# Kernel tuning notes

Hardware: AMD Instinct MI355X
Metric: run time of the kernel (lower is better)

The kernel has to match this reference:

```python
import jax, jax.numpy as jnp
import numpy as np
import jax.lax as lax

B, S, E, H = 8, 4096, 1024, 128
TAU = 1.0
MIN_K = 32

def setup_inputs() -> dict:
    key = jax.random.key(0)
    k0, k1, k2, k3 = jax.random.split(key, 4)
    token_embeddings = jax.random.normal(k0, (B, S, E), dtype=jnp.float32)
    w1 = jax.random.normal(k1, (E, H), dtype=jnp.float32) * (1.0 / np.sqrt(E))
    b1 = jnp.zeros((H,), dtype=jnp.float32)
    w2 = jax.random.normal(k2, (H, 1), dtype=jnp.float32) * (1.0 / np.sqrt(H))
    b2 = jnp.zeros((1,), dtype=jnp.float32)
    # uniform noise for Gumbel, same bounds as the original module
    u = jax.random.uniform(k3, (B, S), minval=1e-08, maxval=1.0 - 1e-08, dtype=jnp.float32)
    return {"token_embeddings": token_embeddings, "w1": w1, "b1": b1, "w2": w2, "b2": b2, "u": u}

def reference(token_embeddings, w1, b1, w2, b2, u):
    # scorer MLP: Dense(H) -> relu -> Dense(1), squeeze -> [B, S]
    h = jax.nn.relu(jnp.einsum('bse,eh->bsh', token_embeddings, w1) + b1)
    importance_logits = (jnp.einsum('bsh,ho->bso', h, w2) + b2)[..., 0]  # [B, S]

    # expected_k (value_function is None): soft count of kept tokens
    expected_k = jax.nn.sigmoid(importance_logits).sum(axis=-1)  # [B]
    k = jnp.clip(expected_k.astype(jnp.int32), MIN_K, None)      # [B]

    # Gumbel-softmax top-k, hard=True
    gumbel = -jnp.log(-jnp.log(u))
    soft_mask = jax.nn.softmax((importance_logits + gumbel) / TAU, axis=-1)  # [B, S]

    # hard mask: 1.0 at the top-k[i] positions of soft_mask per row.
    # Equivalent to the original argsort + while_loop scatter: positions with
    # descending-sort rank < k[i] get 1.0.
    order = jnp.argsort(-soft_mask, axis=-1)          # [B, S] descending order
    ranks = jnp.argsort(order, axis=-1)               # rank of each position
    hard_mask = (ranks < k[:, None]).astype(soft_mask.dtype)

    selection_mask = lax.stop_gradient(hard_mask - soft_mask) + soft_mask
    filtered_embeddings = token_embeddings * selection_mask[..., None]
    return filtered_embeddings, selection_mask, expected_k
```

## Files before the change

kernel.cpp:

```cpp
#include <hip/hip_runtime.h>
#include <hip/hip_bf16.h>
#include <math.h>

#define B_ 8
#define S_ 4096
#define E_ 1024
#define H_ 128
#define MIN_K 32
#define OUT_MASK_OFF (B_*S_*E_)
#define OUT_EK_OFF   (B_*S_*E_ + B_*S_)

#define LOGITS_OFF 0
#define SOFT_OFF   131072
#define CNT_OFF    262144
#define KROW_OFF   393216
#define W1T_HI_OFF 393248
#define W1T_LO_OFF 655392

typedef __attribute__((ext_vector_type(8))) short   frag8;
typedef __attribute__((ext_vector_type(4))) float   fragc;
typedef __attribute__((ext_vector_type(4))) unsigned short us4;

static __device__ __forceinline__ unsigned short bf16_rne(float f) {
  unsigned u = __float_as_uint(f);
  unsigned r = u + 0x7FFF + ((u >> 16) & 1);
  return (unsigned short)(r >> 16);
}
static __device__ __forceinline__ float bf16_to_f32(unsigned short h) {
  return __uint_as_float(((unsigned)h) << 16);
}

__global__ __launch_bounds__(256) void prep_w_kernel(
    const float* __restrict__ w1,
    unsigned short* __restrict__ w1t_hi, unsigned short* __restrict__ w1t_lo)
{
  int id = blockIdx.x * 256 + threadIdx.x;
  int k  = id >> 5;
  int n4 = id & 31;
  float4 w = *(const float4*)(w1 + k * H_ + n4 * 4);
#pragma unroll
  for (int e = 0; e < 4; ++e) {
    float f = (e == 0) ? w.x : (e == 1) ? w.y : (e == 2) ? w.z : w.w;
    unsigned short hi = bf16_rne(f);
    unsigned short lo = bf16_rne(f - bf16_to_f32(hi));
    int n = n4 * 4 + e;
    w1t_hi[n * E_ + k] = hi;
    w1t_lo[n * E_ + k] = lo;
  }
}

#define KT 32
#define XS_STRIDE 40
#define NTILES (E_ / KT)

__global__ __launch_bounds__(256, 4) void scorer_kernel(
    const float* __restrict__ x,
    const unsigned short* __restrict__ w1t_hi,
    const unsigned short* __restrict__ w1t_lo,
    const float* __restrict__ b1, const float* __restrict__ w2,
    const float* __restrict__ b2, float* __restrict__ logits)
{
  __shared__ unsigned short xs_hi[2][32 * XS_STRIDE];
  __shared__ unsigned short xs_lo[2][32 * XS_STRIDE];
  __shared__ float part[4][32];

  const int tid  = threadIdx.x;
  const int wave = tid >> 6;
  const int lane = tid & 63;
  const int l15  = lane & 15;
  const int quad = lane >> 4;
  const int m0   = blockIdx.x * 32;
  const int nbase = wave * 32;

  fragc acc[2][2];
#pragma unroll
  for (int mt = 0; mt < 2; ++mt)
#pragma unroll
    for (int nt = 0; nt < 2; ++nt)
      acc[mt][nt] = (fragc)(0.f);

  const int sm = tid >> 3, skq = tid & 7;
  const float* xrow = x + (size_t)(m0 + sm) * E_ + skq * 4;

  float4 pa = *(const float4*)(xrow);
  float4 pb = *(const float4*)(xrow + KT);

  frag8 bh[2], bl[2], bhn[2], bln[2];
#pragma unroll
  for (int nt = 0; nt < 2; ++nt) {
    int n = nbase + nt * 16 + l15;
    size_t off = (size_t)n * E_ + quad * 8;
    bh[nt] = *(const frag8*)(w1t_hi + off);
    bl[nt] = *(const frag8*)(w1t_lo + off);
  }

#pragma unroll 2
  for (int t = 0; t < NTILES; ++t) {
    const int buf = t & 1;
    {
      us4 h4, l4;
      float fv[4] = {pa.x, pa.y, pa.z, pa.w};
#pragma unroll
      for (int e = 0; e < 4; ++e) {
        unsigned short hi = bf16_rne(fv[e]);
        h4[e] = hi; l4[e] = bf16_rne(fv[e] - bf16_to_f32(hi));
      }
      *(us4*)&xs_hi[buf][sm * XS_STRIDE + skq * 4] = h4;
      *(us4*)&xs_lo[buf][sm * XS_STRIDE + skq * 4] = l4;
    }
    __syncthreads();

    pa = pb;
    if (t + 2 < NTILES)
      pb = *(const float4*)(xrow + (t + 2) * KT);
    if (t + 1 < NTILES) {
#pragma unroll
      for (int nt = 0; nt < 2; ++nt) {
        int n = nbase + nt * 16 + l15;
        size_t off = (size_t)n * E_ + (t + 1) * KT + quad * 8;
        bhn[nt] = *(const frag8*)(w1t_hi + off);
        bln[nt] = *(const frag8*)(w1t_lo + off);
      }
    }

    frag8 ah[2], al[2];
#pragma unroll
    for (int mt = 0; mt < 2; ++mt) {
      int a = (mt * 16 + l15) * XS_STRIDE + quad * 8;
      ah[mt] = *(const frag8*)&xs_hi[buf][a];
      al[mt] = *(const frag8*)&xs_lo[buf][a];
    }
#pragma unroll
    for (int mt = 0; mt < 2; ++mt)
#pragma unroll
      for (int nt = 0; nt < 2; ++nt) {
        acc[mt][nt] = __builtin_amdgcn_mfma_f32_16x16x32_bf16(ah[mt], bh[nt], acc[mt][nt], 0, 0, 0);
        acc[mt][nt] = __builtin_amdgcn_mfma_f32_16x16x32_bf16(ah[mt], bl[nt], acc[mt][nt], 0, 0, 0);
        acc[mt][nt] = __builtin_amdgcn_mfma_f32_16x16x32_bf16(al[mt], bh[nt], acc[mt][nt], 0, 0, 0);
      }
#pragma unroll
    for (int nt = 0; nt < 2; ++nt) { bh[nt] = bhn[nt]; bl[nt] = bln[nt]; }
  }

  float b1v[2], w2v[2];
#pragma unroll
  for (int nt = 0; nt < 2; ++nt) {
    int n = nbase + nt * 16 + l15;
    b1v[nt] = b1[n]; w2v[nt] = w2[n];
  }
  float v[2][4];
#pragma unroll
  for (int mt = 0; mt < 2; ++mt)
#pragma unroll
    for (int reg = 0; reg < 4; ++reg) {
      float p = 0.f;
#pragma unroll
      for (int nt = 0; nt < 2; ++nt) {
        float h = acc[mt][nt][reg] + b1v[nt];
        h = h > 0.f ? h : 0.f;
        p = fmaf(h, w2v[nt], p);
      }
      v[mt][reg] = p;
    }
#pragma unroll
  for (int mask = 1; mask < 16; mask <<= 1)
#pragma unroll
    for (int mt = 0; mt < 2; ++mt)
#pragma unroll
      for (int reg = 0; reg < 4; ++reg)
        v[mt][reg] += __shfl_xor(v[mt][reg], mask);

  if (l15 == 0) {
#pragma unroll
    for (int mt = 0; mt < 2; ++mt)
#pragma unroll
      for (int reg = 0; reg < 4; ++reg)
        part[wave][mt * 16 + quad * 4 + reg] = v[mt][reg];
  }
  __syncthreads();
  if (tid < 32)
    logits[m0 + tid] = ((part[0][tid] + part[1][tid]) + (part[2][tid] + part[3][tid])) + b2[0];
}

__global__ __launch_bounds__(1024) void row_kernel(
    const float* __restrict__ logits, const float* __restrict__ u,
    float* __restrict__ soft, int* __restrict__ krow, float* __restrict__ ek_out)
{
  const int b = blockIdx.x;
  const int t = threadIdx.x;
  const float* Lrow = logits + b * S_;
  const float* urow = u + b * S_;

  __shared__ double red[1024];
  __shared__ float  redf[1024];

  float z[4];
  double psig = 0.0;
  float zmax = -INFINITY;
#pragma unroll
  for (int i = 0; i < 4; ++i) {
    int j = t + i * 1024;
    float L = Lrow[j];
    float g = -logf(-logf(urow[j]));
    z[i] = L + g;
    psig += (double)(1.f / (1.f + expf(-L)));
    zmax = fmaxf(zmax, z[i]);
  }
  red[t] = psig; redf[t] = zmax;
  __syncthreads();
  for (int s2 = 512; s2 > 0; s2 >>= 1) {
    if (t < s2) { red[t] += red[t + s2]; redf[t] = fmaxf(redf[t], redf[t + s2]); }
    __syncthreads();
  }
  __shared__ float m_sh; __shared__ double ek_sh;
  if (t == 0) { m_sh = redf[0]; ek_sh = red[0]; }
  __syncthreads();
  float m = m_sh;

  float e[4];
  double pexp = 0.0;
#pragma unroll
  for (int i = 0; i < 4; ++i) { e[i] = expf(z[i] - m); pexp += (double)e[i]; }
  red[t] = pexp;
  __syncthreads();
  for (int s2 = 512; s2 > 0; s2 >>= 1) {
    if (t < s2) red[t] += red[t + s2];
    __syncthreads();
  }
  __shared__ float den_sh;
  if (t == 0) den_sh = (float)red[0];
  __syncthreads();
  float den = den_sh;
#pragma unroll
  for (int i = 0; i < 4; ++i) soft[b * S_ + t + i * 1024] = e[i] / den;

  if (t == 0) {
    float ekf = (float)ek_sh;
    int k = (int)ekf;
    if (k < MIN_K) k = MIN_K;
    krow[b] = k;
    ek_out[b] = ekf;
  }
}

__global__ __launch_bounds__(256) void rank_kernel(
    const float* __restrict__ soft, int* __restrict__ counts)
{
  __shared__ float4 sjs[256];
  const int b  = blockIdx.z;
  const int ic = blockIdx.x;
  const int jc = blockIdx.y;
  const int tid = threadIdx.x;
  const float* row = soft + b * S_;

  sjs[tid] = ((const float4*)row)[jc * 256 + tid];
  const int i = ic * 256 + tid;
  const float si = row[i];
  __syncthreads();

  int cnt = 0;
  const int jbase = jc * 1024;
  for (int j4 = 0; j4 < 256; ++j4) {
    float4 vv = sjs[j4];
    int j = jbase + j4 * 4;
    cnt += (vv.x > si) || (vv.x == si && (j + 0) < i);
    cnt += (vv.y > si) || (vv.y == si && (j + 1) < i);
    cnt += (vv.z > si) || (vv.z == si && (j + 2) < i);
    cnt += (vv.w > si) || (vv.w == si && (j + 3) < i);
  }
  atomicAdd(&counts[b * S_ + i], cnt);
}

__global__ __launch_bounds__(256) void filter_kernel(
    const float* __restrict__ x, const float* __restrict__ soft,
    const int* __restrict__ counts, const int* __restrict__ krow,
    float* __restrict__ out, float* __restrict__ mask_out)
{
  const int token = blockIdx.x;
  const int b = token >> 12;
  const float s = soft[token];
  const float h = (counts[token] < krow[b]) ? 1.f : 0.f;
  const float sel = (h - s) + s;

  size_t base = (size_t)token * (E_ / 4) + threadIdx.x;
  float4 v = ((const float4*)x)[base];
  v.x *= sel; v.y *= sel; v.z *= sel; v.w *= sel;
  ((float4*)out)[base] = v;
  if (threadIdx.x == 0) mask_out[token] = sel;
}

extern "C" void kernel_launch(void* const* d_in, const int* in_sizes, int n_in,
                              void* d_out, int out_size, void* d_ws, size_t ws_size,
                              hipStream_t stream) {
  const float* x  = (const float*)d_in[0];
  const float* w1 = (const float*)d_in[1];
  const float* b1 = (const float*)d_in[2];
  const float* w2 = (const float*)d_in[3];
  const float* b2 = (const float*)d_in[4];
  const float* u  = (const float*)d_in[5];

  float* out = (float*)d_out;
  float* out_filt = out;
  float* out_mask = out + OUT_MASK_OFF;
  float* out_ek   = out + OUT_EK_OFF;

  char* ws = (char*)d_ws;
  float*          ws_logits = (float*)(ws + LOGITS_OFF);
  float*          ws_soft   = (float*)(ws + SOFT_OFF);
  int*            ws_cnt    = (int*)(ws + CNT_OFF);
  int*            ws_krow   = (int*)(ws + KROW_OFF);
  unsigned short* ws_w1thi  = (unsigned short*)(ws + W1T_HI_OFF);
  unsigned short* ws_w1tlo  = (unsigned short*)(ws + W1T_LO_OFF);

  hipMemsetAsync(ws_cnt, 0, B_ * S_ * sizeof(int), stream);
  prep_w_kernel<<<dim3(128), dim3(256), 0, stream>>>(w1, ws_w1thi, ws_w1tlo);
  scorer_kernel<<<dim3(B_ * S_ / 32), dim3(256), 0, stream>>>(
      x, ws_w1thi, ws_w1tlo, b1, w2, b2, ws_logits);
  row_kernel<<<dim3(B_), dim3(1024), 0, stream>>>(ws_logits, u, ws_soft, ws_krow, out_ek);
  rank_kernel<<<dim3(16, 4, 8), dim3(256), 0, stream>>>(ws_soft, ws_cnt);
  filter_kernel<<<dim3(B_ * S_), dim3(256), 0, stream>>>(
      x, ws_soft, ws_cnt, ws_krow, out_filt, out_mask);
}
```

Baseline: 351.4 us.

## Load scorer A fragments directly to registers and enlarge block tile to 64 rows

The scorer GEMM no longer stages x through shared memory with a per-tile barrier. Each wave loads its own A fragments from global memory into registers, splits them into bf16 hi/lo parts in place, and double-buffers A and B fragments in registers. The block tile grows to 64 rows with a 2x2 wave layout, so each wave computes 32x64 and reuses each B fragment across two M tiles. The aim is to remove LDS traffic and barriers and improve operand reuse, at the cost of more registers (occupancy lowered to 2), redundant hi/lo conversion in each N-half wave, and less coalesced strided global loads for x.

```diff
diff --git a/kernel.cpp b/kernel.cpp
--- a/kernel.cpp
+++ b/kernel.cpp
@@ -19,7 +19,6 @@
 
 typedef __attribute__((ext_vector_type(8))) short   frag8;
 typedef __attribute__((ext_vector_type(4))) float   fragc;
-typedef __attribute__((ext_vector_type(4))) unsigned short us4;
 
 static __device__ __forceinline__ unsigned short bf16_rne(float f) {
   unsigned u = __float_as_uint(f);
@@ -50,105 +49,108 @@
 }
 
 #define KT 32
-#define XS_STRIDE 40
 #define NTILES (E_ / KT)
 
-__global__ __launch_bounds__(256, 4) void scorer_kernel(
+__global__ __launch_bounds__(256, 2) void scorer_kernel(
     const float* __restrict__ x,
     const unsigned short* __restrict__ w1t_hi,
     const unsigned short* __restrict__ w1t_lo,
     const float* __restrict__ b1, const float* __restrict__ w2,
     const float* __restrict__ b2, float* __restrict__ logits)
 {
-  __shared__ unsigned short xs_hi[2][32 * XS_STRIDE];
-  __shared__ unsigned short xs_lo[2][32 * XS_STRIDE];
-  __shared__ float part[4][32];
+  __shared__ float part[2][4][32];
 
   const int tid  = threadIdx.x;
-  const int wave = tid >> 6;
+  const int wv   = tid >> 6;
   const int lane = tid & 63;
   const int l15  = lane & 15;
   const int quad = lane >> 4;
-  const int m0   = blockIdx.x * 32;
-  const int nbase = wave * 32;
-
-  fragc acc[2][2];
+  const int mh   = wv >> 1;
+  const int nh   = wv & 1;
+  const int m0   = blockIdx.x * 64;
+
+  const float* __restrict__ ar[2];
 #pragma unroll
   for (int mt = 0; mt < 2; ++mt)
-#pragma unroll
-    for (int nt = 0; nt < 2; ++nt)
+    ar[mt] = x + (size_t)(m0 + mh * 32 + mt * 16 + l15) * E_ + quad * 8;
+
+  const unsigned short* __restrict__ bhp[4];
+  const unsigned short* __restrict__ blp[4];
+#pragma unroll
+  for (int nt = 0; nt < 4; ++nt) {
+    size_t off = (size_t)(nh * 64 + nt * 16 + l15) * E_ + quad * 8;
+    bhp[nt] = w1t_hi + off;
+    blp[nt] = w1t_lo + off;
+  }
+
+  fragc acc[2][4];
+#pragma unroll
+  for (int mt = 0; mt < 2; ++mt)
+#pragma unroll
+    for (int nt = 0; nt < 4; ++nt)
       acc[mt][nt] = (fragc)(0.f);
 
-  const int sm = tid >> 3, skq = tid & 7;
-  const float* xrow = x + (size_t)(m0 + sm) * E_ + skq * 4;
-
-  float4 pa = *(const float4*)(xrow);
-  float4 pb = *(const float4*)(xrow + KT);
-
-  frag8 bh[2], bl[2], bhn[2], bln[2];
-#pragma unroll
-  for (int nt = 0; nt < 2; ++nt) {
-    int n = nbase + nt * 16 + l15;
-    size_t off = (size_t)n * E_ + quad * 8;
-    bh[nt] = *(const frag8*)(w1t_hi + off);
-    bl[nt] = *(const frag8*)(w1t_lo + off);
+  float4 Ax[2][2][2];
+  frag8  Bh[2][4], Bl[2][4];
+
+#pragma unroll
+  for (int mt = 0; mt < 2; ++mt) {
+    Ax[0][mt][0] = *(const float4*)(ar[mt] + 0);
+    Ax[0][mt][1] = *(const float4*)(ar[mt] + 4);
+  }
+#pragma unroll
+  for (int nt = 0; nt < 4; ++nt) {
+    Bh[0][nt] = *(const frag8*)(bhp[nt]);
+    Bl[0][nt] = *(const frag8*)(blp[nt]);
   }
 
 #pragma unroll 2
   for (int t = 0; t < NTILES; ++t) {
-    const int buf = t & 1;
-    {
-      us4 h4, l4;
-      float fv[4] = {pa.x, pa.y, pa.z, pa.w};
-#pragma unroll
-      for (int e = 0; e < 4; ++e) {
-        unsigned short hi = bf16_rne(fv[e]);
-        h4[e] = hi; l4[e] = bf16_rne(fv[e] - bf16_to_f32(hi));
-      }
-      *(us4*)&xs_hi[buf][sm * XS_STRIDE + skq * 4] = h4;
-      *(us4*)&xs_lo[buf][sm * XS_STRIDE + skq * 4] = l4;
+    const int cur = t & 1;
+    const int nxt = cur ^ 1;
+    const int kn = (t + 1 < NTILES) ? (t + 1) * KT : 0;
+
+#pragma unroll
+    for (int mt = 0; mt < 2; ++mt) {
+      Ax[nxt][mt][0] = *(const float4*)(ar[mt] + kn);
+      Ax[nxt][mt][1] = *(const float4*)(ar[mt] + kn + 4);
     }
-    __syncthreads();
-
-    pa = pb;
-    if (t + 2 < NTILES)
-      pb = *(const float4*)(xrow + (t + 2) * KT);
-    if (t + 1 < NTILES) {
-#pragma unroll
-      for (int nt = 0; nt < 2; ++nt) {
-        int n = nbase + nt * 16 + l15;
-        size_t off = (size_t)n * E_ + (t + 1) * KT + quad * 8;
-        bhn[nt] = *(const frag8*)(w1t_hi + off);
-        bln[nt] = *(const frag8*)(w1t_lo + off);
-      }
+#pragma unroll
+    for (int nt = 0; nt < 4; ++nt) {
+      Bh[nxt][nt] = *(const frag8*)(bhp[nt] + kn);
+      Bl[nxt][nt] = *(const frag8*)(blp[nt] + kn);
     }
 
     frag8 ah[2], al[2];
 #pragma unroll
     for (int mt = 0; mt < 2; ++mt) {
-      int a = (mt * 16 + l15) * XS_STRIDE + quad * 8;
-      ah[mt] = *(const frag8*)&xs_hi[buf][a];
-      al[mt] = *(const frag8*)&xs_lo[buf][a];
+      float f[8] = {Ax[cur][mt][0].x, Ax[cur][mt][0].y, Ax[cur][mt][0].z, Ax[cur][mt][0].w,
+                    Ax[cur][mt][1].x, Ax[cur][mt][1].y, Ax[cur][mt][1].z, Ax[cur][mt][1].w};
+#pragma unroll
+      for (int e = 0; e < 8; ++e) {
+        unsigned short hi = bf16_rne(f[e]);
+        ah[mt][e] = (short)hi;
+        al[mt][e] = (short)bf16_rne(f[e] - bf16_to_f32(hi));
+      }
     }
+
 #pragma unroll
     for (int mt = 0; mt < 2; ++mt)
 #pragma unroll
-      for (int nt = 0; nt < 2; ++nt) {
-        acc[mt][nt] = __builtin_amdgcn_mfma_f32_16x16x32_bf16(ah[mt], bh[nt], acc[mt][nt], 0, 0, 0);
-        acc[mt][nt] = __builtin_amdgcn_mfma_f32_16x16x32_bf16(ah[mt], bl[nt], acc[mt][nt], 0, 0, 0);
-        acc[mt][nt] = __builtin_amdgcn_mfma_f32_16x16x32_bf16(al[mt], bh[nt], acc[mt][nt], 0, 0, 0);
-      }
-#pragma unroll
-    for (int nt = 0; nt < 2; ++nt) { bh[nt] = bhn[nt]; bl[nt] = bln[nt]; }
-  }
-
-  float b1v[2], w2v[2];
-#pragma unroll
-  for (int nt = 0; nt < 2; ++nt) {
-    int n = nbase + nt * 16 + l15;
+      for (int nt = 0; nt < 4; ++nt) {
+        acc[mt][nt] = __builtin_amdgcn_mfma_f32_16x16x32_bf16(ah[mt], Bh[cur][nt], acc[mt][nt], 0, 0, 0);
+        acc[mt][nt] = __builtin_amdgcn_mfma_f32_16x16x32_bf16(ah[mt], Bl[cur][nt], acc[mt][nt], 0, 0, 0);
+        acc[mt][nt] = __builtin_amdgcn_mfma_f32_16x16x32_bf16(al[mt], Bh[cur][nt], acc[mt][nt], 0, 0, 0);
+      }
+  }
+
+  float b1v[4], w2v[4];
+#pragma unroll
+  for (int nt = 0; nt < 4; ++nt) {
+    int n = nh * 64 + nt * 16 + l15;
     b1v[nt] = b1[n]; w2v[nt] = w2[n];
   }
-  float v[2][4];
+  float pA[2][4], pB[2][4];
 #pragma unroll
   for (int mt = 0; mt < 2; ++mt)
 #pragma unroll
@@ -160,26 +162,42 @@
         h = h > 0.f ? h : 0.f;
         p = fmaf(h, w2v[nt], p);
       }
-      v[mt][reg] = p;
+      pA[mt][reg] = p;
+      p = 0.f;
+#pragma unroll
+      for (int nt = 2; nt < 4; ++nt) {
+        float h = acc[mt][nt][reg] + b1v[nt];
+        h = h > 0.f ? h : 0.f;
+        p = fmaf(h, w2v[nt], p);
+      }
+      pB[mt][reg] = p;
     }
 #pragma unroll
   for (int mask = 1; mask < 16; mask <<= 1)
 #pragma unroll
     for (int mt = 0; mt < 2; ++mt)
 #pragma unroll
-      for (int reg = 0; reg < 4; ++reg)
-        v[mt][reg] += __shfl_xor(v[mt][reg], mask);
+      for (int reg = 0; reg < 4; ++reg) {
+        pA[mt][reg] += __shfl_xor(pA[mt][reg], mask);
+        pB[mt][reg] += __shfl_xor(pB[mt][reg], mask);
+      }
 
   if (l15 == 0) {
 #pragma unroll
     for (int mt = 0; mt < 2; ++mt)
 #pragma unroll
-      for (int reg = 0; reg < 4; ++reg)
-        part[wave][mt * 16 + quad * 4 + reg] = v[mt][reg];
-  }
-  __syncthreads();
-  if (tid < 32)
-    logits[m0 + tid] = ((part[0][tid] + part[1][tid]) + (part[2][tid] + part[3][tid])) + b2[0];
+      for (int reg = 0; reg < 4; ++reg) {
+        int rl = mt * 16 + quad * 4 + reg;
+        part[mh][nh * 2 + 0][rl] = pA[mt][reg];
+        part[mh][nh * 2 + 1][rl] = pB[mt][reg];
+      }
+  }
+  __syncthreads();
+  if (tid < 64) {
+    int rmh = tid >> 5, rl = tid & 31;
+    logits[m0 + tid] = ((part[rmh][0][rl] + part[rmh][1][rl]) +
+                        (part[rmh][2][rl] + part[rmh][3][rl])) + b2[0];
+  }
 }
 
 __global__ __launch_bounds__(1024) void row_kernel(
@@ -314,7 +332,7 @@
 
   hipMemsetAsync(ws_cnt, 0, B_ * S_ * sizeof(int), stream);
   prep_w_kernel<<<dim3(128), dim3(256), 0, stream>>>(w1, ws_w1thi, ws_w1tlo);
-  scorer_kernel<<<dim3(B_ * S_ / 32), dim3(256), 0, stream>>>(
+  scorer_kernel<<<dim3(B_ * S_ / 64), dim3(256), 0, stream>>>(
       x, ws_w1thi, ws_w1tlo, b1, w2, b2, ws_logits);
   row_kernel<<<dim3(B_), dim3(1024), 0, stream>>>(ws_logits, u, ws_soft, ws_krow, out_ek);
   rank_kernel<<<dim3(16, 4, 8), dim3(256), 0, stream>>>(ws_soft, ws_cnt);
```

New measurement: 382.0 us. 1.09x slower.

## Load A fragments directly from global memory, drop LDS staging and barriers

Applied to the files above, without the earlier changes.

The scorer kernel no longer stages the fp32 embedding tile through double-buffered shared memory. Each wave now loads its own A fragments straight from global memory into registers and splits them into bf16 hi/lo parts there, which removes the per-tile __syncthreads and the LDS write/read traffic. The explicit register prefetch of the next tile is also dropped in favour of a simple non-unrolled loop. In exchange, all four waves redundantly load and convert the same 32x1024 x tile (4x global/L2 traffic and conversion work), and latency hiding now relies on occupancy rather than software pipelining.

```diff
diff --git a/kernel.cpp b/kernel.cpp
--- a/kernel.cpp
+++ b/kernel.cpp
@@ -19,7 +19,6 @@
 
 typedef __attribute__((ext_vector_type(8))) short   frag8;
 typedef __attribute__((ext_vector_type(4))) float   fragc;
-typedef __attribute__((ext_vector_type(4))) unsigned short us4;
 
 static __device__ __forceinline__ unsigned short bf16_rne(float f) {
   unsigned u = __float_as_uint(f);
@@ -50,7 +49,6 @@
 }
 
 #define KT 32
-#define XS_STRIDE 40
 #define NTILES (E_ / KT)
 
 __global__ __launch_bounds__(256, 4) void scorer_kernel(
@@ -60,108 +58,83 @@
     const float* __restrict__ b1, const float* __restrict__ w2,
     const float* __restrict__ b2, float* __restrict__ logits)
 {
-  __shared__ unsigned short xs_hi[2][32 * XS_STRIDE];
-  __shared__ unsigned short xs_lo[2][32 * XS_STRIDE];
   __shared__ float part[4][32];
 
   const int tid  = threadIdx.x;
-  const int wave = tid >> 6;
+  const int nh   = tid >> 6;
   const int lane = tid & 63;
   const int l15  = lane & 15;
   const int quad = lane >> 4;
   const int m0   = blockIdx.x * 32;
-  const int nbase = wave * 32;
-
-  fragc acc[2][2];
-#pragma unroll
-  for (int mt = 0; mt < 2; ++mt)
-#pragma unroll
-    for (int nt = 0; nt < 2; ++nt)
-      acc[mt][nt] = (fragc)(0.f);
-
-  const int sm = tid >> 3, skq = tid & 7;
-  const float* xrow = x + (size_t)(m0 + sm) * E_ + skq * 4;
-
-  float4 pa = *(const float4*)(xrow);
-  float4 pb = *(const float4*)(xrow + KT);
-
-  frag8 bh[2], bl[2], bhn[2], bln[2];
-#pragma unroll
-  for (int nt = 0; nt < 2; ++nt) {
-    int n = nbase + nt * 16 + l15;
-    size_t off = (size_t)n * E_ + quad * 8;
-    bh[nt] = *(const frag8*)(w1t_hi + off);
-    bl[nt] = *(const frag8*)(w1t_lo + off);
-  }
-
-#pragma unroll 2
+
+  const float* __restrict__ ar0 = x + (size_t)(m0 + 0  + l15) * E_ + quad * 8;
+  const float* __restrict__ ar1 = x + (size_t)(m0 + 16 + l15) * E_ + quad * 8;
+
+  const size_t bo0 = (size_t)(nh * 32 + 0  + l15) * E_ + quad * 8;
+  const size_t bo1 = (size_t)(nh * 32 + 16 + l15) * E_ + quad * 8;
+  const unsigned short* __restrict__ bh0p = w1t_hi + bo0;
+  const unsigned short* __restrict__ bh1p = w1t_hi + bo1;
+  const unsigned short* __restrict__ bl0p = w1t_lo + bo0;
+  const unsigned short* __restrict__ bl1p = w1t_lo + bo1;
+
+  fragc acc00 = (fragc)(0.f), acc01 = (fragc)(0.f);
+  fragc acc10 = (fragc)(0.f), acc11 = (fragc)(0.f);
+
+#pragma unroll 1
   for (int t = 0; t < NTILES; ++t) {
-    const int buf = t & 1;
+    const int k = t * KT;
+
+    float4 a00 = *(const float4*)(ar0 + k);
+    float4 a01 = *(const float4*)(ar0 + k + 4);
+    float4 a10 = *(const float4*)(ar1 + k);
+    float4 a11 = *(const float4*)(ar1 + k + 4);
+    frag8 bh0 = *(const frag8*)(bh0p + k);
+    frag8 bh1 = *(const frag8*)(bh1p + k);
+    frag8 bl0 = *(const frag8*)(bl0p + k);
+    frag8 bl1 = *(const frag8*)(bl1p + k);
+
+    frag8 ah0, al0, ah1, al1;
     {
-      us4 h4, l4;
-      float fv[4] = {pa.x, pa.y, pa.z, pa.w};
-#pragma unroll
-      for (int e = 0; e < 4; ++e) {
-        unsigned short hi = bf16_rne(fv[e]);
-        h4[e] = hi; l4[e] = bf16_rne(fv[e] - bf16_to_f32(hi));
-      }
-      *(us4*)&xs_hi[buf][sm * XS_STRIDE + skq * 4] = h4;
-      *(us4*)&xs_lo[buf][sm * XS_STRIDE + skq * 4] = l4;
-    }
-    __syncthreads();
-
-    pa = pb;
-    if (t + 2 < NTILES)
-      pb = *(const float4*)(xrow + (t + 2) * KT);
-    if (t + 1 < NTILES) {
-#pragma unroll
-      for (int nt = 0; nt < 2; ++nt) {
-        int n = nbase + nt * 16 + l15;
-        size_t off = (size_t)n * E_ + (t + 1) * KT + quad * 8;
-        bhn[nt] = *(const frag8*)(w1t_hi + off);
-        bln[nt] = *(const frag8*)(w1t_lo + off);
+      float f0[8] = {a00.x, a00.y, a00.z, a00.w, a01.x, a01.y, a01.z, a01.w};
+      float f1[8] = {a10.x, a10.y, a10.z, a10.w, a11.x, a11.y, a11.z, a11.w};
+#pragma unroll
+      for (int e = 0; e < 8; ++e) {
+        unsigned short hi0 = bf16_rne(f0[e]);
+        ah0[e] = (short)hi0;
+        al0[e] = (short)bf16_rne(f0[e] - bf16_to_f32(hi0));
+        unsigned short hi1 = bf16_rne(f1[e]);
+        ah1[e] = (short)hi1;
+        al1[e] = (short)bf16_rne(f1[e] - bf16_to_f32(hi1));
       }
     }
 
-    frag8 ah[2], al[2];
-#pragma unroll
-    for (int mt = 0; mt < 2; ++mt) {
-      int a = (mt * 16 + l15) * XS_STRIDE + quad * 8;
-      ah[mt] = *(const frag8*)&xs_hi[buf][a];
-      al[mt] = *(const frag8*)&xs_lo[buf][a];
-    }
-#pragma unroll
-    for (int mt = 0; mt < 2; ++mt)
-#pragma unroll
-      for (int nt = 0; nt < 2; ++nt) {
-        acc[mt][nt] = __builtin_amdgcn_mfma_f32_16x16x32_bf16(ah[mt], bh[nt], acc[mt][nt], 0, 0, 0);
-        acc[mt][nt] = __builtin_amdgcn_mfma_f32_16x16x32_bf16(ah[mt], bl[nt], acc[mt][nt], 0, 0, 0);
-        acc[mt][nt] = __builtin_amdgcn_mfma_f32_16x16x32_bf16(al[mt], bh[nt], acc[mt][nt], 0, 0, 0);
-      }
-#pragma unroll
-    for (int nt = 0; nt < 2; ++nt) { bh[nt] = bhn[nt]; bl[nt] = bln[nt]; }
-  }
-
-  float b1v[2], w2v[2];
-#pragma unroll
-  for (int nt = 0; nt < 2; ++nt) {
-    int n = nbase + nt * 16 + l15;
-    b1v[nt] = b1[n]; w2v[nt] = w2[n];
-  }
+    acc00 = __builtin_amdgcn_mfma_f32_16x16x32_bf16(ah0, bh0, acc00, 0, 0, 0);
+    acc00 = __builtin_amdgcn_mfma_f32_16x16x32_bf16(ah0, bl0, acc00, 0, 0, 0);
+    acc00 = __builtin_amdgcn_mfma_f32_16x16x32_bf16(al0, bh0, acc00, 0, 0, 0);
+    acc01 = __builtin_amdgcn_mfma_f32_16x16x32_bf16(ah0, bh1, acc01, 0, 0, 0);
+    acc01 = __builtin_amdgcn_mfma_f32_16x16x32_bf16(ah0, bl1, acc01, 0, 0, 0);
+    acc01 = __builtin_amdgcn_mfma_f32_16x16x32_bf16(al0, bh1, acc01, 0, 0, 0);
+    acc10 = __builtin_amdgcn_mfma_f32_16x16x32_bf16(ah1, bh0, acc10, 0, 0, 0);
+    acc10 = __builtin_amdgcn_mfma_f32_16x16x32_bf16(ah1, bl0, acc10, 0, 0, 0);
+    acc10 = __builtin_amdgcn_mfma_f32_16x16x32_bf16(al1, bh0, acc10, 0, 0, 0);
+    acc11 = __builtin_amdgcn_mfma_f32_16x16x32_bf16(ah1, bh1, acc11, 0, 0, 0);
+    acc11 = __builtin_amdgcn_mfma_f32_16x16x32_bf16(ah1, bl1, acc11, 0, 0, 0);
+    acc11 = __builtin_amdgcn_mfma_f32_16x16x32_bf16(al1, bh1, acc11, 0, 0, 0);
+  }
+
+  float b1v0 = b1[nh * 32 + 0  + l15], w2v0 = w2[nh * 32 + 0  + l15];
+  float b1v1 = b1[nh * 32 + 16 + l15], w2v1 = w2[nh * 32 + 16 + l15];
+
   float v[2][4];
 #pragma unroll
-  for (int mt = 0; mt < 2; ++mt)
-#pragma unroll
-    for (int reg = 0; reg < 4; ++reg) {
-      float p = 0.f;
-#pragma unroll
-      for (int nt = 0; nt < 2; ++nt) {
-        float h = acc[mt][nt][reg] + b1v[nt];
-        h = h > 0.f ? h : 0.f;
-        p = fmaf(h, w2v[nt], p);
-      }
-      v[mt][reg] = p;
-    }
+  for (int reg = 0; reg < 4; ++reg) {
+    float h0 = acc00[reg] + b1v0; h0 = h0 > 0.f ? h0 : 0.f;
+    float h1 = acc01[reg] + b1v1; h1 = h1 > 0.f ? h1 : 0.f;
+    v[0][reg] = fmaf(h1, w2v1, fmaf(h0, w2v0, 0.f));
+    float g0 = acc10[reg] + b1v0; g0 = g0 > 0.f ? g0 : 0.f;
+    float g1 = acc11[reg] + b1v1; g1 = g1 > 0.f ? g1 : 0.f;
+    v[1][reg] = fmaf(g1, w2v1, fmaf(g0, w2v0, 0.f));
+  }
 #pragma unroll
   for (int mask = 1; mask < 16; mask <<= 1)
 #pragma unroll
@@ -175,11 +148,12 @@
     for (int mt = 0; mt < 2; ++mt)
 #pragma unroll
       for (int reg = 0; reg < 4; ++reg)
-        part[wave][mt * 16 + quad * 4 + reg] = v[mt][reg];
+        part[nh][mt * 16 + quad * 4 + reg] = v[mt][reg];
   }
   __syncthreads();
   if (tid < 32)
-    logits[m0 + tid] = ((part[0][tid] + part[1][tid]) + (part[2][tid] + part[3][tid])) + b2[0];
+    logits[m0 + tid] = ((part[0][tid] + part[1][tid]) +
+                        (part[2][tid] + part[3][tid])) + b2[0];
 }
 
 __global__ __launch_bounds__(1024) void row_kernel(
```

Result: slower. 391.7 us (+11.5%).

## Retile scorer GEMM to 128-row blocks with shared-memory staged W1 tiles

Applied to the files above, without the earlier changes.

The scorer kernel now processes 128 token rows per 512-thread block instead of 32 rows per 256 threads. W1 is pre-packed into per-K-tile contiguous hi/lo bf16 blocks and staged through double-buffered shared memory, so each block reads it once per tile instead of every wave reading it from global memory. The goal is to cut redundant W1 traffic, since W1 per block is amortized over 4x more rows, and to improve MFMA density per wave (2x4 tiles). In exchange, LDS use rises to about 80KB per block, occupancy drops, and the loop is not unrolled.

```diff
diff --git a/kernel.cpp b/kernel.cpp
--- a/kernel.cpp
+++ b/kernel.cpp
@@ -14,12 +14,10 @@
 #define SOFT_OFF   131072
 #define CNT_OFF    262144
 #define KROW_OFF   393216
-#define W1T_HI_OFF 393248
-#define W1T_LO_OFF 655392
+#define WB_OFF     393248
 
 typedef __attribute__((ext_vector_type(8))) short   frag8;
 typedef __attribute__((ext_vector_type(4))) float   fragc;
-typedef __attribute__((ext_vector_type(4))) unsigned short us4;
 
 static __device__ __forceinline__ unsigned short bf16_rne(float f) {
   unsigned u = __float_as_uint(f);
@@ -31,121 +29,141 @@
 }
 
 __global__ __launch_bounds__(256) void prep_w_kernel(
-    const float* __restrict__ w1,
-    unsigned short* __restrict__ w1t_hi, unsigned short* __restrict__ w1t_lo)
+    const float* __restrict__ w1, unsigned short* __restrict__ wb)
 {
   int id = blockIdx.x * 256 + threadIdx.x;
   int k  = id >> 5;
   int n4 = id & 31;
   float4 w = *(const float4*)(w1 + k * H_ + n4 * 4);
+  int t  = k >> 5;
+  int kp = k & 31;
 #pragma unroll
   for (int e = 0; e < 4; ++e) {
     float f = (e == 0) ? w.x : (e == 1) ? w.y : (e == 2) ? w.z : w.w;
     unsigned short hi = bf16_rne(f);
     unsigned short lo = bf16_rne(f - bf16_to_f32(hi));
     int n = n4 * 4 + e;
-    w1t_hi[n * E_ + k] = hi;
-    w1t_lo[n * E_ + k] = lo;
+    wb[t * 8192 +        n * 32 + kp] = hi;
+    wb[t * 8192 + 4096 + n * 32 + kp] = lo;
   }
 }
 
 #define KT 32
-#define XS_STRIDE 40
 #define NTILES (E_ / KT)
-
-__global__ __launch_bounds__(256, 4) void scorer_kernel(
+#define XS 40
+
+__global__ __launch_bounds__(512, 2) void scorer_kernel(
     const float* __restrict__ x,
-    const unsigned short* __restrict__ w1t_hi,
-    const unsigned short* __restrict__ w1t_lo,
+    const unsigned short* __restrict__ wb,
     const float* __restrict__ b1, const float* __restrict__ w2,
     const float* __restrict__ b2, float* __restrict__ logits)
 {
-  __shared__ unsigned short xs_hi[2][32 * XS_STRIDE];
-  __shared__ unsigned short xs_lo[2][32 * XS_STRIDE];
-  __shared__ float part[4][32];
+  __shared__ unsigned short as_hi[2][128 * XS];
+  __shared__ unsigned short as_lo[2][128 * XS];
+  __shared__ unsigned short bs_hi[2][128 * XS];
+  __shared__ unsigned short bs_lo[2][128 * XS];
+  __shared__ float part[2][128];
 
   const int tid  = threadIdx.x;
-  const int wave = tid >> 6;
+  const int wv   = tid >> 6;
   const int lane = tid & 63;
   const int l15  = lane & 15;
   const int quad = lane >> 4;
-  const int m0   = blockIdx.x * 32;
-  const int nbase = wave * 32;
-
-  fragc acc[2][2];
+  const int mg   = wv >> 1;
+  const int ng   = wv & 1;
+  const int m0   = blockIdx.x * 128;
+
+  const int r = tid >> 2, p = tid & 3;
+  const float* __restrict__ xsrc = x + (size_t)(m0 + r) * E_ + p * 8;
+  const unsigned short* __restrict__ bsrc = wb + tid * 16;
+  const int bplane = tid >> 8;
+  const int boff   = ((tid >> 1) & 127) * XS + (tid & 1) * 16;
+  const int aoff   = r * XS + p * 8;
+
+  fragc acc[2][4];
 #pragma unroll
   for (int mt = 0; mt < 2; ++mt)
 #pragma unroll
-    for (int nt = 0; nt < 2; ++nt)
+    for (int nt = 0; nt < 4; ++nt)
       acc[mt][nt] = (fragc)(0.f);
 
-  const int sm = tid >> 3, skq = tid & 7;
-  const float* xrow = x + (size_t)(m0 + sm) * E_ + skq * 4;
-
-  float4 pa = *(const float4*)(xrow);
-  float4 pb = *(const float4*)(xrow + KT);
-
-  frag8 bh[2], bl[2], bhn[2], bln[2];
-#pragma unroll
-  for (int nt = 0; nt < 2; ++nt) {
-    int n = nbase + nt * 16 + l15;
-    size_t off = (size_t)n * E_ + quad * 8;
-    bh[nt] = *(const frag8*)(w1t_hi + off);
-    bl[nt] = *(const frag8*)(w1t_lo + off);
-  }
-
-#pragma unroll 2
+  float4 a0 = *(const float4*)(xsrc);
+  float4 a1 = *(const float4*)(xsrc + 4);
+  uint4  q0 = *(const uint4*)(bsrc);
+  uint4  q1 = *(const uint4*)(bsrc + 8);
+  {
+    frag8 h8, l8;
+    float f[8] = {a0.x, a0.y, a0.z, a0.w, a1.x, a1.y, a1.z, a1.w};
+#pragma unroll
+    for (int e = 0; e < 8; ++e) {
+      unsigned short hi = bf16_rne(f[e]);
+      h8[e] = (short)hi; l8[e] = (short)bf16_rne(f[e] - bf16_to_f32(hi));
+    }
+    *(frag8*)&as_hi[0][aoff] = h8;
+    *(frag8*)&as_lo[0][aoff] = l8;
+    unsigned short* bd = bplane ? &bs_lo[0][boff] : &bs_hi[0][boff];
+    *(uint4*)(bd) = q0;
+    *(uint4*)(bd + 8) = q1;
+  }
+  __syncthreads();
+
+#pragma unroll 1
   for (int t = 0; t < NTILES; ++t) {
     const int buf = t & 1;
-    {
-      us4 h4, l4;
-      float fv[4] = {pa.x, pa.y, pa.z, pa.w};
-#pragma unroll
-      for (int e = 0; e < 4; ++e) {
-        unsigned short hi = bf16_rne(fv[e]);
-        h4[e] = hi; l4[e] = bf16_rne(fv[e] - bf16_to_f32(hi));
-      }
-      *(us4*)&xs_hi[buf][sm * XS_STRIDE + skq * 4] = h4;
-      *(us4*)&xs_lo[buf][sm * XS_STRIDE + skq * 4] = l4;
-    }
-    __syncthreads();
-
-    pa = pb;
-    if (t + 2 < NTILES)
-      pb = *(const float4*)(xrow + (t + 2) * KT);
-    if (t + 1 < NTILES) {
-#pragma unroll
-      for (int nt = 0; nt < 2; ++nt) {
-        int n = nbase + nt * 16 + l15;
-        size_t off = (size_t)n * E_ + (t + 1) * KT + quad * 8;
-        bhn[nt] = *(const frag8*)(w1t_hi + off);
-        bln[nt] = *(const frag8*)(w1t_lo + off);
-      }
-    }
-
-    frag8 ah[2], al[2];
+    const bool more = (t + 1 < NTILES);
+
+    float4 na0, na1; uint4 nq0, nq1;
+    if (more) {
+      na0 = *(const float4*)(xsrc + (t + 1) * KT);
+      na1 = *(const float4*)(xsrc + (t + 1) * KT + 4);
+      nq0 = *(const uint4*)(bsrc + (t + 1) * 8192);
+      nq1 = *(const uint4*)(bsrc + (t + 1) * 8192 + 8);
+    }
+
+    frag8 ah[2], al[2], bh[4], bl[4];
 #pragma unroll
     for (int mt = 0; mt < 2; ++mt) {
-      int a = (mt * 16 + l15) * XS_STRIDE + quad * 8;
-      ah[mt] = *(const frag8*)&xs_hi[buf][a];
-      al[mt] = *(const frag8*)&xs_lo[buf][a];
-    }
+      int a = (mg * 32 + mt * 16 + l15) * XS + quad * 8;
+      ah[mt] = *(const frag8*)&as_hi[buf][a];
+      al[mt] = *(const frag8*)&as_lo[buf][a];
+    }
+#pragma unroll
+    for (int nt = 0; nt < 4; ++nt) {
+      int a = (ng * 64 + nt * 16 + l15) * XS + quad * 8;
+      bh[nt] = *(const frag8*)&bs_hi[buf][a];
+      bl[nt] = *(const frag8*)&bs_lo[buf][a];
+    }
+
 #pragma unroll
     for (int mt = 0; mt < 2; ++mt)
 #pragma unroll
-      for (int nt = 0; nt < 2; ++nt) {
+      for (int nt = 0; nt < 4; ++nt) {
         acc[mt][nt] = __builtin_amdgcn_mfma_f32_16x16x32_bf16(ah[mt], bh[nt], acc[mt][nt], 0, 0, 0);
         acc[mt][nt] = __builtin_amdgcn_mfma_f32_16x16x32_bf16(ah[mt], bl[nt], acc[mt][nt], 0, 0, 0);
         acc[mt][nt] = __builtin_amdgcn_mfma_f32_16x16x32_bf16(al[mt], bh[nt], acc[mt][nt], 0, 0, 0);
       }
-#pragma unroll
-    for (int nt = 0; nt < 2; ++nt) { bh[nt] = bhn[nt]; bl[nt] = bln[nt]; }
-  }
-
-  float b1v[2], w2v[2];
-#pragma unroll
-  for (int nt = 0; nt < 2; ++nt) {
-    int n = nbase + nt * 16 + l15;
+
+    if (more) {
+      frag8 h8, l8;
+      float f[8] = {na0.x, na0.y, na0.z, na0.w, na1.x, na1.y, na1.z, na1.w};
+#pragma unroll
+      for (int e = 0; e < 8; ++e) {
+        unsigned short hi = bf16_rne(f[e]);
+        h8[e] = (short)hi; l8[e] = (short)bf16_rne(f[e] - bf16_to_f32(hi));
+      }
+      *(frag8*)&as_hi[buf ^ 1][aoff] = h8;
+      *(frag8*)&as_lo[buf ^ 1][aoff] = l8;
+      unsigned short* bd = bplane ? &bs_lo[buf ^ 1][boff] : &bs_hi[buf ^ 1][boff];
+      *(uint4*)(bd) = nq0;
+      *(uint4*)(bd + 8) = nq1;
+    }
+    __syncthreads();
+  }
+
+  float b1v[4], w2v[4];
+#pragma unroll
+  for (int nt = 0; nt < 4; ++nt) {
+    int n = ng * 64 + nt * 16 + l15;
     b1v[nt] = b1[n]; w2v[nt] = w2[n];
   }
   float v[2][4];
@@ -153,14 +171,14 @@
   for (int mt = 0; mt < 2; ++mt)
 #pragma unroll
     for (int reg = 0; reg < 4; ++reg) {
-      float p = 0.f;
-#pragma unroll
-      for (int nt = 0; nt < 2; ++nt) {
+      float pacc = 0.f;
+#pragma unroll
+      for (int nt = 0; nt < 4; ++nt) {
         float h = acc[mt][nt][reg] + b1v[nt];
         h = h > 0.f ? h : 0.f;
-        p = fmaf(h, w2v[nt], p);
+        pacc = fmaf(h, w2v[nt], pacc);
       }
-      v[mt][reg] = p;
+      v[mt][reg] = pacc;
     }
 #pragma unroll
   for (int mask = 1; mask < 16; mask <<= 1)
@@ -175,11 +193,11 @@
     for (int mt = 0; mt < 2; ++mt)
 #pragma unroll
       for (int reg = 0; reg < 4; ++reg)
-        part[wave][mt * 16 + quad * 4 + reg] = v[mt][reg];
-  }
-  __syncthreads();
-  if (tid < 32)
-    logits[m0 + tid] = ((part[0][tid] + part[1][tid]) + (part[2][tid] + part[3][tid])) + b2[0];
+        part[ng][mg * 32 + mt * 16 + quad * 4 + reg] = v[mt][reg];
+  }
+  __syncthreads();
+  if (tid < 128)
+    logits[m0 + tid] = (part[0][tid] + part[1][tid]) + b2[0];
 }
 
 __global__ __launch_bounds__(1024) void row_kernel(
@@ -309,13 +327,12 @@
   float*          ws_soft   = (float*)(ws + SOFT_OFF);
   int*            ws_cnt    = (int*)(ws + CNT_OFF);
   int*            ws_krow   = (int*)(ws + KROW_OFF);
-  unsigned short* ws_w1thi  = (unsigned short*)(ws + W1T_HI_OFF);
-  unsigned short* ws_w1tlo  = (unsigned short*)(ws + W1T_LO_OFF);
+  unsigned short* ws_wb     = (unsigned short*)(ws + WB_OFF);
 
   hipMemsetAsync(ws_cnt, 0, B_ * S_ * sizeof(int), stream);
-  prep_w_kernel<<<dim3(128), dim3(256), 0, stream>>>(w1, ws_w1thi, ws_w1tlo);
-  scorer_kernel<<<dim3(B_ * S_ / 32), dim3(256), 0, stream>>>(
-      x, ws_w1thi, ws_w1tlo, b1, w2, b2, ws_logits);
+  prep_w_kernel<<<dim3(128), dim3(256), 0, stream>>>(w1, ws_wb);
+  scorer_kernel<<<dim3(B_ * S_ / 128), dim3(512), 0, stream>>>(
+      x, ws_wb, b1, w2, b2, ws_logits);
   row_kernel<<<dim3(B_), dim3(1024), 0, stream>>>(ws_logits, u, ws_soft, ws_krow, out_ek);
   rank_kernel<<<dim3(16, 4, 8), dim3(256), 0, stream>>>(ws_soft, ws_cnt);
   filter_kernel<<<dim3(B_ * S_), dim3(256), 0, stream>>>(
```

Measured after the change: 313.8 us. -10.7%, faster.
